# Kernel optimization log

Measured on AMD Instinct MI355X. Metric: run time of the kernel, lower is better.

The kernel has to match this reference:

```python
import jax, jax.numpy as jnp
import numpy as np

N = 50000      # num_nodes
E = 12500      # num hyperedges
NNZ = 400000   # incidence pairs
OBS = 64
LAT = 64
STEPS = 20     # (t1 - t0) / dt = 1.0 / 0.05
DT = 0.05
SQRT_DT = DT ** 0.5
SIGMA_INIT = 0.1


def setup_inputs() -> dict:
    key = jax.random.key(0)
    ks = jax.random.split(key, 12)
    w = lambda k, o, i: jax.random.normal(k, (o, i), dtype=jnp.float32) * (1.0 / np.sqrt(i))
    return {
        "x": jax.random.normal(ks[0], (N, OBS), dtype=jnp.float32),
        "enc_w1": w(ks[1], LAT, OBS),
        "enc_b1": jnp.zeros((LAT,), jnp.float32),
        "enc_w2": w(ks[2], LAT, LAT),
        "enc_b2": jnp.zeros((LAT,), jnp.float32),
        "conv_w": w(ks[3], LAT, LAT),
        "conv_b": jnp.zeros((LAT,), jnp.float32),
        "sigma": SIGMA_INIT * jnp.ones((LAT,), jnp.float32),
        "dec_w1": w(ks[4], LAT, LAT),
        "dec_b1": jnp.zeros((LAT,), jnp.float32),
        "dec_w2": w(ks[5], OBS, LAT),
        "dec_b2": jnp.zeros((OBS,), jnp.float32),
        "node_idx": jax.random.randint(ks[6], (NNZ,), 0, N),
        "edge_idx": jax.random.randint(ks[7], (NNZ,), 0, E),
        "seed": 0,
    }


def _mlp(x, w1, b1, w2, b2):
    # eqx.nn.MLP depth=1: linear -> relu -> linear, applied per node (vmapped == matmul)
    return jax.nn.relu(x @ w1.T + b1) @ w2.T + b2


def reference(x, enc_w1, enc_b1, enc_w2, enc_b2, conv_w, conv_b, sigma,
              dec_w1, dec_b1, dec_w2, dec_b2, node_idx, edge_idx, seed):
    # incidence degree normalization (HGNN-style), computed once
    ones = jnp.ones((NNZ,), jnp.float32)
    edge_deg_inv = 1.0 / jnp.maximum(jax.ops.segment_sum(ones, edge_idx, num_segments=E), 1.0)
    node_deg_inv = 1.0 / jnp.maximum(jax.ops.segment_sum(ones, node_idx, num_segments=N), 1.0)

    def conv(y):
        m = y @ conv_w.T                                                    # [N, LAT]
        e = jax.ops.segment_sum(m[node_idx], edge_idx, num_segments=E)     # node -> hyperedge
        e = e * edge_deg_inv[:, None]
        out = jax.ops.segment_sum(e[edge_idx], node_idx, num_segments=N)   # hyperedge -> node
        return out * node_deg_inv[:, None] + conv_b

    def step(y, k):
        dw = jax.random.normal(k, (N, LAT), dtype=y.dtype)
        drift = jnp.tanh(conv(y))                       # activation(conv) drift
        y = y + drift * DT + sigma * SQRT_DT * dw       # Euler-Maruyama, diagonal noise
        return y, None

    z0 = _mlp(x, enc_w1, enc_b1, enc_w2, enc_b2)        # encode (n, obs) -> (n, lat)
    keys = jax.random.split(jax.random.key(seed), STEPS)
    z1, _ = jax.lax.scan(step, z0, keys)
    return _mlp(z1, dec_w1, dec_b1, dec_w2, dec_b2)     # decode at t1
```

## Files before the change

kernel.cpp:

```cpp
#include <hip/hip_runtime.h>
#include <stdint.h>

#define N_NODES 50000
#define N_EDGES 12500
#define NNZV    400000
#define STEPS   20
#define DT_F    0.05f
#define SQRTDT_F 0.22360679774997896f

__device__ __forceinline__ float rdlf(float v, int l) {
  return __uint_as_float(__builtin_amdgcn_readlane(__float_as_uint(v), (unsigned)l));
}
__device__ __forceinline__ int rdli(int v, int l) {
  return (int)__builtin_amdgcn_readlane((unsigned)v, (unsigned)l);
}

__device__ __forceinline__ void tf2x32(uint32_t k0, uint32_t k1,
                                       uint32_t x0, uint32_t x1,
                                       uint32_t& o0, uint32_t& o1) {
  uint32_t k2 = k0 ^ k1 ^ 0x1BD11BDAu;
#define TFR(r) { x0 += x1; x1 = (x1 << (r)) | (x1 >> (32 - (r))); x1 ^= x0; }
  x0 += k0; x1 += k1;
  TFR(13) TFR(15) TFR(26) TFR(6)   x0 += k1; x1 += k2 + 1u;
  TFR(17) TFR(29) TFR(16) TFR(24)  x0 += k2; x1 += k0 + 2u;
  TFR(13) TFR(15) TFR(26) TFR(6)   x0 += k0; x1 += k1 + 3u;
  TFR(17) TFR(29) TFR(16) TFR(24)  x0 += k1; x1 += k2 + 4u;
  TFR(13) TFR(15) TFR(26) TFR(6)   x0 += k2; x1 += k0 + 5u;
#undef TFR
  o0 = x0; o1 = x1;
}

__device__ __forceinline__ float erfinv_xla(float x) {
  float w = -log1pf(-x * x);
  float p;
  if (w < 5.0f) {
    w = w - 2.5f;
    p =              2.81022636e-08f;
    p = fmaf(p, w,   3.43273939e-07f);
    p = fmaf(p, w,  -3.5233877e-06f);
    p = fmaf(p, w,  -4.39150654e-06f);
    p = fmaf(p, w,   0.00021858087f);
    p = fmaf(p, w,  -0.00125372503f);
    p = fmaf(p, w,  -0.00417768164f);
    p = fmaf(p, w,   0.246640727f);
    p = fmaf(p, w,   1.50140941f);
  } else {
    w = sqrtf(w) - 3.0f;
    p =             -0.000200214257f;
    p = fmaf(p, w,   0.000100950558f);
    p = fmaf(p, w,   0.00134934322f);
    p = fmaf(p, w,  -0.00367342844f);
    p = fmaf(p, w,   0.00573950773f);
    p = fmaf(p, w,  -0.0076224613f);
    p = fmaf(p, w,   0.00943887047f);
    p = fmaf(p, w,   1.00167406f);
    p = fmaf(p, w,   2.83297682f);
  }
  return p * x;
}

__device__ __forceinline__ float bits_to_normal(uint32_t b) {
  float f = __uint_as_float((b >> 9) | 0x3f800000u) - 1.0f;
  const float lo = -0.99999994f;
  float u = fmaf(f, 2.0f, lo);
  u = fmaxf(u, lo);
  return 1.41421356237f * erfinv_xla(u);
}

__global__ void k_keys(const int* __restrict__ seed, unsigned* __restrict__ keys) {
  int j = threadIdx.x;
  if (j < STEPS) {
    unsigned s = (unsigned)seed[0];
    unsigned o0, o1;
    tf2x32(0u, s, 0u, (unsigned)j, o0, o1);
    keys[2 * j] = o0; keys[2 * j + 1] = o1;
  }
}

__global__ void k_zero(int* __restrict__ p, int n) {
  int i = blockIdx.x * 256 + threadIdx.x;
  if (i < n) p[i] = 0;
}

__global__ void k_hist(const int* __restrict__ nidx, const int* __restrict__ eidx,
                       int* __restrict__ ecnt, int* __restrict__ ncnt) {
  int i = blockIdx.x * 256 + threadIdx.x;
  if (i < NNZV) {
    atomicAdd(&ecnt[eidx[i]], 1);
    atomicAdd(&ncnt[nidx[i]], 1);
  }
}

__global__ __launch_bounds__(256) void k_reduce(const int* __restrict__ cnt, int len,
                                                int* __restrict__ bsum) {
  __shared__ int sh[256];
  int b = blockIdx.x, tid = threadIdx.x;
  int base = b * 1024 + tid * 4;
  int s = 0;
#pragma unroll
  for (int j = 0; j < 4; ++j) {
    int i = base + j;
    if (i < len) s += cnt[i];
  }
  sh[tid] = s;
  __syncthreads();
  for (int off = 128; off > 0; off >>= 1) {
    if (tid < off) sh[tid] += sh[tid + off];
    __syncthreads();
  }
  if (tid == 0) bsum[b] = sh[0];
}

__global__ __launch_bounds__(256) void k_scanb(int* __restrict__ bsum, int nb) {
  __shared__ int sh[256];
  int tid = threadIdx.x;
  int v = (tid < nb) ? bsum[tid] : 0;
  sh[tid] = v;
  __syncthreads();
  for (int off = 1; off < 256; off <<= 1) {
    int t = (tid >= off) ? sh[tid - off] : 0;
    __syncthreads();
    sh[tid] += t;
    __syncthreads();
  }
  if (tid < nb) bsum[tid] = sh[tid] - v;
}

__global__ __launch_bounds__(256) void k_scatter(const int* __restrict__ cnt,
                                                 const int* __restrict__ bsum, int len,
                                                 int* __restrict__ start,
                                                 int* __restrict__ fill,
                                                 float* __restrict__ dinv) {
  __shared__ int sh[256];
  int b = blockIdx.x, tid = threadIdx.x;
  int base = b * 1024 + tid * 4;
  int c[4], lex[4];
  int s = 0;
#pragma unroll
  for (int j = 0; j < 4; ++j) {
    int i = base + j;
    c[j] = (i < len) ? cnt[i] : 0;
    lex[j] = s;
    s += c[j];
  }
  sh[tid] = s;
  __syncthreads();
  for (int off = 1; off < 256; off <<= 1) {
    int t = (tid >= off) ? sh[tid - off] : 0;
    __syncthreads();
    sh[tid] += t;
    __syncthreads();
  }
  int off0 = bsum[b] + sh[tid] - s;
#pragma unroll
  for (int j = 0; j < 4; ++j) {
    int i = base + j;
    if (i < len) {
      start[i] = off0 + lex[j];
      fill[i] = 0;
      dinv[i] = 1.0f / (float)(c[j] > 1 ? c[j] : 1);
    }
  }
}

__global__ void k_fill(const int* __restrict__ nidx, const int* __restrict__ eidx,
                       const int* __restrict__ estart, const int* __restrict__ nstart,
                       int* __restrict__ efill, int* __restrict__ nfill,
                       int* __restrict__ emem, int* __restrict__ nmem) {
  int i = blockIdx.x * 256 + threadIdx.x;
  if (i < NNZV) {
    int e = eidx[i], n = nidx[i];
    int pe = atomicAdd(&efill[e], 1);
    emem[estart[e] + pe] = n;
    int pn = atomicAdd(&nfill[n], 1);
    nmem[nstart[n] + pn] = e;
  }
}

__device__ __forceinline__ void stage_swz(const float* __restrict__ w,
                                          float* __restrict__ lds, int tid) {
  for (int idx = tid; idx < 4096; idx += 256) {
    int j = idx >> 6, k = idx & 63;
    lds[k * 64 + (j ^ k)] = w[idx];
  }
}

__device__ __forceinline__ float seg_gather_sum(const float* __restrict__ rows,
                                                const int* __restrict__ mem,
                                                int start, int deg, int lane) {
  float acc0 = 0.f, acc1 = 0.f;
  for (int base = 0; base < deg; base += 64) {
    int rem = min(64, deg - base);
    int ids = (lane < rem) ? mem[start + base + lane] : 0;
    int i = 0;
    for (; i + 8 <= rem; i += 8) {
      int i0 = rdli(ids, i),     i1 = rdli(ids, i + 1);
      int i2 = rdli(ids, i + 2), i3 = rdli(ids, i + 3);
      int i4 = rdli(ids, i + 4), i5 = rdli(ids, i + 5);
      int i6 = rdli(ids, i + 6), i7 = rdli(ids, i + 7);
      float v0 = rows[(size_t)i0 * 64 + lane], v1 = rows[(size_t)i1 * 64 + lane];
      float v2 = rows[(size_t)i2 * 64 + lane], v3 = rows[(size_t)i3 * 64 + lane];
      float v4 = rows[(size_t)i4 * 64 + lane], v5 = rows[(size_t)i5 * 64 + lane];
      float v6 = rows[(size_t)i6 * 64 + lane], v7 = rows[(size_t)i7 * 64 + lane];
      acc0 += (v0 + v1) + (v2 + v3);
      acc1 += (v4 + v5) + (v6 + v7);
    }
    for (; i + 4 <= rem; i += 4) {
      int i0 = rdli(ids, i),     i1 = rdli(ids, i + 1);
      int i2 = rdli(ids, i + 2), i3 = rdli(ids, i + 3);
      float v0 = rows[(size_t)i0 * 64 + lane], v1 = rows[(size_t)i1 * 64 + lane];
      float v2 = rows[(size_t)i2 * 64 + lane], v3 = rows[(size_t)i3 * 64 + lane];
      acc0 += (v0 + v1) + (v2 + v3);
    }
    for (; i < rem; ++i) acc0 += rows[(size_t)rdli(ids, i) * 64 + lane];
  }
  return acc0 + acc1;
}

__global__ __launch_bounds__(256) void k_encoder(
    const float* __restrict__ x, const float* __restrict__ w1,
    const float* __restrict__ b1, const float* __restrict__ w2,
    const float* __restrict__ b2, float* __restrict__ y) {
  __shared__ float lw1[4096], lw2[4096];
  int tid = threadIdx.x;
  stage_swz(w1, lw1, tid);
  stage_swz(w2, lw2, tid);
  __syncthreads();
  int lane = tid & 63, wave = tid >> 6;
  float w1r[64], w2r[64];
#pragma unroll
  for (int k = 0; k < 64; ++k) {
    w1r[k] = lw1[k * 64 + (lane ^ k)];
    w2r[k] = lw2[k * 64 + (lane ^ k)];
  }
  float b1v = b1[lane], b2v = b2[lane];
  int gw = blockIdx.x * 4 + wave, nw = gridDim.x * 4;
  for (int n = gw; n < N_NODES; n += nw) {
    float xv = x[(size_t)n * 64 + lane];
    float a0 = 0.f, a1 = 0.f, a2 = 0.f, a3 = 0.f;
#pragma unroll
    for (int k = 0; k < 64; k += 4) {
      a0 = fmaf(rdlf(xv, k),     w1r[k],     a0);
      a1 = fmaf(rdlf(xv, k + 1), w1r[k + 1], a1);
      a2 = fmaf(rdlf(xv, k + 2), w1r[k + 2], a2);
      a3 = fmaf(rdlf(xv, k + 3), w1r[k + 3], a3);
    }
    float h = fmaxf((a0 + a1) + (a2 + a3) + b1v, 0.f);
    a0 = a1 = a2 = a3 = 0.f;
#pragma unroll
    for (int k = 0; k < 64; k += 4) {
      a0 = fmaf(rdlf(h, k),     w2r[k],     a0);
      a1 = fmaf(rdlf(h, k + 1), w2r[k + 1], a1);
      a2 = fmaf(rdlf(h, k + 2), w2r[k + 2], a2);
      a3 = fmaf(rdlf(h, k + 3), w2r[k + 3], a3);
    }
    y[(size_t)n * 64 + lane] = (a0 + a1) + (a2 + a3) + b2v;
  }
}

__global__ __launch_bounds__(256) void k_edge(
    const float* __restrict__ y, float* __restrict__ e,
    const int* __restrict__ estart, const int* __restrict__ ecnt,
    const int* __restrict__ emem, const float* __restrict__ edinv,
    const float* __restrict__ cw) {
  __shared__ float lcw[4096];
  int tid = threadIdx.x;
  stage_swz(cw, lcw, tid);
  __syncthreads();
  int lane = tid & 63, wave = tid >> 6;
  float cwr[64];
#pragma unroll
  for (int k = 0; k < 64; ++k) cwr[k] = lcw[k * 64 + (lane ^ k)];
  int gw = blockIdx.x * 4 + wave, nw = gridDim.x * 4;
  for (int ed = gw; ed < N_EDGES; ed += nw) {
    int start = estart[ed], deg = ecnt[ed];
    float acc = seg_gather_sum(y, emem, start, deg, lane);
    float a0 = 0.f, a1 = 0.f, a2 = 0.f, a3 = 0.f;
#pragma unroll
    for (int k = 0; k < 64; k += 4) {
      a0 = fmaf(rdlf(acc, k),     cwr[k],     a0);
      a1 = fmaf(rdlf(acc, k + 1), cwr[k + 1], a1);
      a2 = fmaf(rdlf(acc, k + 2), cwr[k + 2], a2);
      a3 = fmaf(rdlf(acc, k + 3), cwr[k + 3], a3);
    }
    e[(size_t)ed * 64 + lane] = ((a0 + a1) + (a2 + a3)) * edinv[ed];
  }
}

__global__ __launch_bounds__(256) void k_node(
    const float* __restrict__ e, float* __restrict__ y,
    const int* __restrict__ nstart, const int* __restrict__ ncnt,
    const int* __restrict__ nmem, const float* __restrict__ ndinv,
    const float* __restrict__ cb, const float* __restrict__ sigma,
    const unsigned* __restrict__ keys, int s) {
  int tid = threadIdx.x;
  int lane = tid & 63, wave = tid >> 6;
  float cbv = cb[lane];
  float sgv = sigma[lane] * SQRTDT_F;
  unsigned ka = keys[2 * s], kb = keys[2 * s + 1];
  int gw = blockIdx.x * 4 + wave, nw = gridDim.x * 4;
  for (int n = gw; n < N_NODES; n += nw) {
    uint32_t r0, r1;
    tf2x32(ka, kb, 0u, (unsigned)(n * 64 + lane), r0, r1);
    float dw = bits_to_normal(r0 ^ r1);
    float acc = seg_gather_sum(e, nmem, nstart[n], ncnt[n], lane);
    float yv = y[(size_t)n * 64 + lane];
    yv = yv + tanhf(fmaf(acc, ndinv[n], cbv)) * DT_F + sgv * dw;
    y[(size_t)n * 64 + lane] = yv;
  }
}

__global__ __launch_bounds__(256) void k_decoder(
    const float* __restrict__ y, const float* __restrict__ w1,
    const float* __restrict__ b1, const float* __restrict__ w2,
    const float* __restrict__ b2, float* __restrict__ out) {
  __shared__ float lw1[4096], lw2[4096];
  int tid = threadIdx.x;
  stage_swz(w1, lw1, tid);
  stage_swz(w2, lw2, tid);
  __syncthreads();
  int lane = tid & 63, wave = tid >> 6;
  float w1r[64], w2r[64];
#pragma unroll
  for (int k = 0; k < 64; ++k) {
    w1r[k] = lw1[k * 64 + (lane ^ k)];
    w2r[k] = lw2[k * 64 + (lane ^ k)];
  }
  float b1v = b1[lane], b2v = b2[lane];
  int gw = blockIdx.x * 4 + wave, nw = gridDim.x * 4;
  for (int n = gw; n < N_NODES; n += nw) {
    float xv = y[(size_t)n * 64 + lane];
    float a0 = 0.f, a1 = 0.f, a2 = 0.f, a3 = 0.f;
#pragma unroll
    for (int k = 0; k < 64; k += 4) {
      a0 = fmaf(rdlf(xv, k),     w1r[k],     a0);
      a1 = fmaf(rdlf(xv, k + 1), w1r[k + 1], a1);
      a2 = fmaf(rdlf(xv, k + 2), w1r[k + 2], a2);
      a3 = fmaf(rdlf(xv, k + 3), w1r[k + 3], a3);
    }
    float h = fmaxf((a0 + a1) + (a2 + a3) + b1v, 0.f);
    a0 = a1 = a2 = a3 = 0.f;
#pragma unroll
    for (int k = 0; k < 64; k += 4) {
      a0 = fmaf(rdlf(h, k),     w2r[k],     a0);
      a1 = fmaf(rdlf(h, k + 1), w2r[k + 1], a1);
      a2 = fmaf(rdlf(h, k + 2), w2r[k + 2], a2);
      a3 = fmaf(rdlf(h, k + 3), w2r[k + 3], a3);
    }
    out[(size_t)n * 64 + lane] = (a0 + a1) + (a2 + a3) + b2v;
  }
}

extern "C" void kernel_launch(void* const* d_in, const int* in_sizes, int n_in,
                              void* d_out, int out_size, void* d_ws, size_t ws_size,
                              hipStream_t stream) {
  (void)in_sizes; (void)n_in; (void)out_size; (void)ws_size;
  const float* x      = (const float*)d_in[0];
  const float* enc_w1 = (const float*)d_in[1];
  const float* enc_b1 = (const float*)d_in[2];
  const float* enc_w2 = (const float*)d_in[3];
  const float* enc_b2 = (const float*)d_in[4];
  const float* conv_w = (const float*)d_in[5];
  const float* conv_b = (const float*)d_in[6];
  const float* sigma  = (const float*)d_in[7];
  const float* dec_w1 = (const float*)d_in[8];
  const float* dec_b1 = (const float*)d_in[9];
  const float* dec_w2 = (const float*)d_in[10];
  const float* dec_b2 = (const float*)d_in[11];
  const int* node_idx = (const int*)d_in[12];
  const int* edge_idx = (const int*)d_in[13];
  const int* seed     = (const int*)d_in[14];

  char* wsb = (char*)d_ws;
  size_t off = 0;
  auto alloc = [&](size_t bytes) -> void* {
    void* p = wsb + off;
    off = (off + bytes + 255) & ~(size_t)255;
    return p;
  };
  float* y        = (float*)alloc((size_t)N_NODES * 64 * 4);
  float* e        = (float*)alloc((size_t)N_EDGES * 64 * 4);
  int* edge_cnt   = (int*)alloc((size_t)N_EDGES * 4);
  int* node_cnt   = (int*)alloc((size_t)N_NODES * 4);
  int* edge_start = (int*)alloc((size_t)N_EDGES * 4);
  int* node_start = (int*)alloc((size_t)N_NODES * 4);
  int* edge_fill  = (int*)alloc((size_t)N_EDGES * 4);
  int* node_fill  = (int*)alloc((size_t)N_NODES * 4);
  int* edge_mem   = (int*)alloc((size_t)NNZV * 4);
  int* node_mem   = (int*)alloc((size_t)NNZV * 4);
  float* edinv    = (float*)alloc((size_t)N_EDGES * 4);
  float* ndinv    = (float*)alloc((size_t)N_NODES * 4);
  unsigned* keys  = (unsigned*)alloc(2 * STEPS * 4);
  int* ebsum      = (int*)alloc(256 * 4);
  int* nbsum      = (int*)alloc(256 * 4);

  const int EB = (N_EDGES + 1023) / 1024;
  const int NB = (N_NODES + 1023) / 1024;

  dim3 b256(256);
  hipLaunchKernelGGL(k_keys, dim3(1), dim3(64), 0, stream, seed, keys);
  hipLaunchKernelGGL(k_zero, dim3((N_EDGES + 255) / 256), b256, 0, stream, edge_cnt, N_EDGES);
  hipLaunchKernelGGL(k_zero, dim3((N_NODES + 255) / 256), b256, 0, stream, node_cnt, N_NODES);
  hipLaunchKernelGGL(k_hist, dim3((NNZV + 255) / 256), b256, 0, stream,
                     node_idx, edge_idx, edge_cnt, node_cnt);
  hipLaunchKernelGGL(k_reduce, dim3(EB), b256, 0, stream, edge_cnt, N_EDGES, ebsum);
  hipLaunchKernelGGL(k_reduce, dim3(NB), b256, 0, stream, node_cnt, N_NODES, nbsum);
  hipLaunchKernelGGL(k_scanb, dim3(1), b256, 0, stream, ebsum, EB);
  hipLaunchKernelGGL(k_scanb, dim3(1), b256, 0, stream, nbsum, NB);
  hipLaunchKernelGGL(k_scatter, dim3(EB), b256, 0, stream,
                     edge_cnt, ebsum, N_EDGES, edge_start, edge_fill, edinv);
  hipLaunchKernelGGL(k_scatter, dim3(NB), b256, 0, stream,
                     node_cnt, nbsum, N_NODES, node_start, node_fill, ndinv);
  hipLaunchKernelGGL(k_fill, dim3((NNZV + 255) / 256), b256, 0, stream,
                     node_idx, edge_idx, edge_start, node_start,
                     edge_fill, node_fill, edge_mem, node_mem);
  hipLaunchKernelGGL(k_encoder, dim3(1024), b256, 0, stream,
                     x, enc_w1, enc_b1, enc_w2, enc_b2, y);
  for (int s = 0; s < STEPS; ++s) {
    hipLaunchKernelGGL(k_edge, dim3(1024), b256, 0, stream,
                       y, e, edge_start, edge_cnt, edge_mem, edinv, conv_w);
    hipLaunchKernelGGL(k_node, dim3(2048), b256, 0, stream,
                       e, y, node_start, node_cnt, node_mem, ndinv,
                       conv_b, sigma, keys, s);
  }
  hipLaunchKernelGGL(k_decoder, dim3(1024), b256, 0, stream,
                     y, dec_w1, dec_b1, dec_w2, dec_b2, (float*)d_out);
}
```

Baseline: 1.210 ms.

## Use fast intrinsics for erfinv/tanh, unroll gather 16-wide, reorder node loads

Swaps log1pf and tanhf for __logf/__expf-based approximations in the noise and drift paths. Widens the gather unroll from 8 to 16 loads with four accumulators to keep more memory requests in flight. Moves the y load and neighbor gather ahead of the RNG compute in k_node so memory latency can overlap the Threefry and erfinv arithmetic. The fast math may slightly change the normal samples and drift compared with the reference, and the wider unroll raises register pressure.

```diff
diff --git a/kernel.cpp b/kernel.cpp
--- a/kernel.cpp
+++ b/kernel.cpp
@@ -30,8 +30,8 @@
   o0 = x0; o1 = x1;
 }
 
-__device__ __forceinline__ float erfinv_xla(float x) {
-  float w = -log1pf(-x * x);
+__device__ __forceinline__ float erfinv_fast(float x) {
+  float w = -__logf((1.0f - x) * (1.0f + x));
   float p;
   if (w < 5.0f) {
     w = w - 2.5f;
@@ -64,7 +64,12 @@
   const float lo = -0.99999994f;
   float u = fmaf(f, 2.0f, lo);
   u = fmaxf(u, lo);
-  return 1.41421356237f * erfinv_xla(u);
+  return 1.41421356237f * erfinv_fast(u);
+}
+
+__device__ __forceinline__ float fast_tanhf(float x) {
+  float t = __expf(2.0f * x);
+  return 1.0f - 2.0f / (t + 1.0f);
 }
 
 __global__ void k_keys(const int* __restrict__ seed, unsigned* __restrict__ keys) {
@@ -188,33 +193,43 @@
 __device__ __forceinline__ float seg_gather_sum(const float* __restrict__ rows,
                                                 const int* __restrict__ mem,
                                                 int start, int deg, int lane) {
-  float acc0 = 0.f, acc1 = 0.f;
+  float acc0 = 0.f, acc1 = 0.f, acc2 = 0.f, acc3 = 0.f;
   for (int base = 0; base < deg; base += 64) {
     int rem = min(64, deg - base);
     int ids = (lane < rem) ? mem[start + base + lane] : 0;
     int i = 0;
-    for (; i + 8 <= rem; i += 8) {
-      int i0 = rdli(ids, i),     i1 = rdli(ids, i + 1);
-      int i2 = rdli(ids, i + 2), i3 = rdli(ids, i + 3);
-      int i4 = rdli(ids, i + 4), i5 = rdli(ids, i + 5);
-      int i6 = rdli(ids, i + 6), i7 = rdli(ids, i + 7);
-      float v0 = rows[(size_t)i0 * 64 + lane], v1 = rows[(size_t)i1 * 64 + lane];
-      float v2 = rows[(size_t)i2 * 64 + lane], v3 = rows[(size_t)i3 * 64 + lane];
-      float v4 = rows[(size_t)i4 * 64 + lane], v5 = rows[(size_t)i5 * 64 + lane];
-      float v6 = rows[(size_t)i6 * 64 + lane], v7 = rows[(size_t)i7 * 64 + lane];
+    for (; i + 16 <= rem; i += 16) {
+      int j0  = rdli(ids, i),      j1  = rdli(ids, i + 1);
+      int j2  = rdli(ids, i + 2),  j3  = rdli(ids, i + 3);
+      int j4  = rdli(ids, i + 4),  j5  = rdli(ids, i + 5);
+      int j6  = rdli(ids, i + 6),  j7  = rdli(ids, i + 7);
+      int j8  = rdli(ids, i + 8),  j9  = rdli(ids, i + 9);
+      int j10 = rdli(ids, i + 10), j11 = rdli(ids, i + 11);
+      int j12 = rdli(ids, i + 12), j13 = rdli(ids, i + 13);
+      int j14 = rdli(ids, i + 14), j15 = rdli(ids, i + 15);
+      float v0  = rows[(size_t)j0  * 64 + lane], v1  = rows[(size_t)j1  * 64 + lane];
+      float v2  = rows[(size_t)j2  * 64 + lane], v3  = rows[(size_t)j3  * 64 + lane];
+      float v4  = rows[(size_t)j4  * 64 + lane], v5  = rows[(size_t)j5  * 64 + lane];
+      float v6  = rows[(size_t)j6  * 64 + lane], v7  = rows[(size_t)j7  * 64 + lane];
+      float v8  = rows[(size_t)j8  * 64 + lane], v9  = rows[(size_t)j9  * 64 + lane];
+      float v10 = rows[(size_t)j10 * 64 + lane], v11 = rows[(size_t)j11 * 64 + lane];
+      float v12 = rows[(size_t)j12 * 64 + lane], v13 = rows[(size_t)j13 * 64 + lane];
+      float v14 = rows[(size_t)j14 * 64 + lane], v15 = rows[(size_t)j15 * 64 + lane];
       acc0 += (v0 + v1) + (v2 + v3);
       acc1 += (v4 + v5) + (v6 + v7);
+      acc2 += (v8 + v9) + (v10 + v11);
+      acc3 += (v12 + v13) + (v14 + v15);
     }
     for (; i + 4 <= rem; i += 4) {
-      int i0 = rdli(ids, i),     i1 = rdli(ids, i + 1);
-      int i2 = rdli(ids, i + 2), i3 = rdli(ids, i + 3);
-      float v0 = rows[(size_t)i0 * 64 + lane], v1 = rows[(size_t)i1 * 64 + lane];
-      float v2 = rows[(size_t)i2 * 64 + lane], v3 = rows[(size_t)i3 * 64 + lane];
+      int j0 = rdli(ids, i),     j1 = rdli(ids, i + 1);
+      int j2 = rdli(ids, i + 2), j3 = rdli(ids, i + 3);
+      float v0 = rows[(size_t)j0 * 64 + lane], v1 = rows[(size_t)j1 * 64 + lane];
+      float v2 = rows[(size_t)j2 * 64 + lane], v3 = rows[(size_t)j3 * 64 + lane];
       acc0 += (v0 + v1) + (v2 + v3);
     }
     for (; i < rem; ++i) acc0 += rows[(size_t)rdli(ids, i) * 64 + lane];
   }
-  return acc0 + acc1;
+  return (acc0 + acc1) + (acc2 + acc3);
 }
 
 __global__ __launch_bounds__(256) void k_encoder(
@@ -300,12 +315,12 @@
   unsigned ka = keys[2 * s], kb = keys[2 * s + 1];
   int gw = blockIdx.x * 4 + wave, nw = gridDim.x * 4;
   for (int n = gw; n < N_NODES; n += nw) {
+    float yv = y[(size_t)n * 64 + lane];
+    float acc = seg_gather_sum(e, nmem, nstart[n], ncnt[n], lane);
     uint32_t r0, r1;
     tf2x32(ka, kb, 0u, (unsigned)(n * 64 + lane), r0, r1);
     float dw = bits_to_normal(r0 ^ r1);
-    float acc = seg_gather_sum(e, nmem, nstart[n], ncnt[n], lane);
-    float yv = y[(size_t)n * 64 + lane];
-    yv = yv + tanhf(fmaf(acc, ndinv[n], cbv)) * DT_F + sgv * dw;
+    yv = fmaf(fast_tanhf(fmaf(acc, ndinv[n], cbv)), DT_F, fmaf(sgv, dw, yv));
     y[(size_t)n * 64 + lane] = yv;
   }
 }
```

Result: slower. 1.437 ms (+18.7%).

## Use scalar index loads in gathers, fast transcendentals, LDS weights, larger edge grid

Applied to the files above, without the earlier changes.

The segment gather now makes the row index wave-uniform with readfirstlane and reads neighbour indices as scalar loads, replacing the per-lane index load followed by readlane. In the edge kernel the 64-register conv weight copy is dropped and weights are read from LDS on each use, which lowers register pressure, and the edge grid is doubled. The node update switches to a fast exp-based tanh and a __logf-based erfinv, and hoists per-node loads ahead of the RNG. These approximations can move results slightly away from the reference, and the LDS reads add shared-memory traffic inside the inner product.

```diff
diff --git a/kernel.cpp b/kernel.cpp
--- a/kernel.cpp
+++ b/kernel.cpp
@@ -11,8 +11,8 @@
 __device__ __forceinline__ float rdlf(float v, int l) {
   return __uint_as_float(__builtin_amdgcn_readlane(__float_as_uint(v), (unsigned)l));
 }
-__device__ __forceinline__ int rdli(int v, int l) {
-  return (int)__builtin_amdgcn_readlane((unsigned)v, (unsigned)l);
+__device__ __forceinline__ int rfl(int v) {
+  return (int)__builtin_amdgcn_readfirstlane((unsigned)v);
 }
 
 __device__ __forceinline__ void tf2x32(uint32_t k0, uint32_t k1,
@@ -30,8 +30,8 @@
   o0 = x0; o1 = x1;
 }
 
-__device__ __forceinline__ float erfinv_xla(float x) {
-  float w = -log1pf(-x * x);
+__device__ __forceinline__ float erfinv_fast(float x) {
+  float w = -__logf((1.0f - x) * (1.0f + x));
   float p;
   if (w < 5.0f) {
     w = w - 2.5f;
@@ -64,7 +64,12 @@
   const float lo = -0.99999994f;
   float u = fmaf(f, 2.0f, lo);
   u = fmaxf(u, lo);
-  return 1.41421356237f * erfinv_xla(u);
+  return 1.41421356237f * erfinv_fast(u);
+}
+
+__device__ __forceinline__ float fast_tanhf(float x) {
+  float t = __expf(2.0f * x);
+  return 1.0f - 2.0f / (t + 1.0f);
 }
 
 __global__ void k_keys(const int* __restrict__ seed, unsigned* __restrict__ keys) {
@@ -185,36 +190,25 @@
   }
 }
 
-__device__ __forceinline__ float seg_gather_sum(const float* __restrict__ rows,
-                                                const int* __restrict__ mem,
-                                                int start, int deg, int lane) {
-  float acc0 = 0.f, acc1 = 0.f;
-  for (int base = 0; base < deg; base += 64) {
-    int rem = min(64, deg - base);
-    int ids = (lane < rem) ? mem[start + base + lane] : 0;
-    int i = 0;
-    for (; i + 8 <= rem; i += 8) {
-      int i0 = rdli(ids, i),     i1 = rdli(ids, i + 1);
-      int i2 = rdli(ids, i + 2), i3 = rdli(ids, i + 3);
-      int i4 = rdli(ids, i + 4), i5 = rdli(ids, i + 5);
-      int i6 = rdli(ids, i + 6), i7 = rdli(ids, i + 7);
-      float v0 = rows[(size_t)i0 * 64 + lane], v1 = rows[(size_t)i1 * 64 + lane];
-      float v2 = rows[(size_t)i2 * 64 + lane], v3 = rows[(size_t)i3 * 64 + lane];
-      float v4 = rows[(size_t)i4 * 64 + lane], v5 = rows[(size_t)i5 * 64 + lane];
-      float v6 = rows[(size_t)i6 * 64 + lane], v7 = rows[(size_t)i7 * 64 + lane];
-      acc0 += (v0 + v1) + (v2 + v3);
-      acc1 += (v4 + v5) + (v6 + v7);
-    }
-    for (; i + 4 <= rem; i += 4) {
-      int i0 = rdli(ids, i),     i1 = rdli(ids, i + 1);
-      int i2 = rdli(ids, i + 2), i3 = rdli(ids, i + 3);
-      float v0 = rows[(size_t)i0 * 64 + lane], v1 = rows[(size_t)i1 * 64 + lane];
-      float v2 = rows[(size_t)i2 * 64 + lane], v3 = rows[(size_t)i3 * 64 + lane];
-      acc0 += (v0 + v1) + (v2 + v3);
-    }
-    for (; i < rem; ++i) acc0 += rows[(size_t)rdli(ids, i) * 64 + lane];
-  }
-  return acc0 + acc1;
+__device__ __forceinline__ float seg_gather_scalar(const float* __restrict__ rows,
+                                                   const int* __restrict__ mem,
+                                                   int st, int deg, int lane) {
+  float a0 = 0.f, a1 = 0.f, a2 = 0.f, a3 = 0.f;
+  int i = 0;
+  for (; i + 8 <= deg; i += 8) {
+    int d0 = mem[st + i],     d1 = mem[st + i + 1];
+    int d2 = mem[st + i + 2], d3 = mem[st + i + 3];
+    int d4 = mem[st + i + 4], d5 = mem[st + i + 5];
+    int d6 = mem[st + i + 6], d7 = mem[st + i + 7];
+    float v0 = rows[(size_t)d0 * 64 + lane], v1 = rows[(size_t)d1 * 64 + lane];
+    float v2 = rows[(size_t)d2 * 64 + lane], v3 = rows[(size_t)d3 * 64 + lane];
+    float v4 = rows[(size_t)d4 * 64 + lane], v5 = rows[(size_t)d5 * 64 + lane];
+    float v6 = rows[(size_t)d6 * 64 + lane], v7 = rows[(size_t)d7 * 64 + lane];
+    a0 += v0 + v1; a1 += v2 + v3; a2 += v4 + v5; a3 += v6 + v7;
+  }
+  for (; i < deg; ++i)
+    a0 += rows[(size_t)mem[st + i] * 64 + lane];
+  return (a0 + a1) + (a2 + a3);
 }
 
 __global__ __launch_bounds__(256) void k_encoder(
@@ -268,22 +262,21 @@
   stage_swz(cw, lcw, tid);
   __syncthreads();
   int lane = tid & 63, wave = tid >> 6;
-  float cwr[64];
-#pragma unroll
-  for (int k = 0; k < 64; ++k) cwr[k] = lcw[k * 64 + (lane ^ k)];
   int gw = blockIdx.x * 4 + wave, nw = gridDim.x * 4;
   for (int ed = gw; ed < N_EDGES; ed += nw) {
-    int start = estart[ed], deg = ecnt[ed];
-    float acc = seg_gather_sum(y, emem, start, deg, lane);
+    int edu = rfl(ed);
+    int st  = estart[edu], deg = ecnt[edu];
+    float div = edinv[edu];
+    float acc = seg_gather_scalar(y, emem, st, deg, lane);
     float a0 = 0.f, a1 = 0.f, a2 = 0.f, a3 = 0.f;
 #pragma unroll
     for (int k = 0; k < 64; k += 4) {
-      a0 = fmaf(rdlf(acc, k),     cwr[k],     a0);
-      a1 = fmaf(rdlf(acc, k + 1), cwr[k + 1], a1);
-      a2 = fmaf(rdlf(acc, k + 2), cwr[k + 2], a2);
-      a3 = fmaf(rdlf(acc, k + 3), cwr[k + 3], a3);
-    }
-    e[(size_t)ed * 64 + lane] = ((a0 + a1) + (a2 + a3)) * edinv[ed];
+      a0 = fmaf(rdlf(acc, k),     lcw[k * 64 + (lane ^ k)],             a0);
+      a1 = fmaf(rdlf(acc, k + 1), lcw[(k + 1) * 64 + (lane ^ (k + 1))], a1);
+      a2 = fmaf(rdlf(acc, k + 2), lcw[(k + 2) * 64 + (lane ^ (k + 2))], a2);
+      a3 = fmaf(rdlf(acc, k + 3), lcw[(k + 3) * 64 + (lane ^ (k + 3))], a3);
+    }
+    e[(size_t)edu * 64 + lane] = ((a0 + a1) + (a2 + a3)) * div;
   }
 }
 
@@ -300,13 +293,16 @@
   unsigned ka = keys[2 * s], kb = keys[2 * s + 1];
   int gw = blockIdx.x * 4 + wave, nw = gridDim.x * 4;
   for (int n = gw; n < N_NODES; n += nw) {
+    int nu = rfl(n);
+    int st = nstart[nu], deg = ncnt[nu];
+    float dinv = ndinv[nu];
+    float yv = y[(size_t)nu * 64 + lane];
+    float acc = seg_gather_scalar(e, nmem, st, deg, lane);
     uint32_t r0, r1;
-    tf2x32(ka, kb, 0u, (unsigned)(n * 64 + lane), r0, r1);
+    tf2x32(ka, kb, 0u, (unsigned)(nu * 64 + lane), r0, r1);
     float dw = bits_to_normal(r0 ^ r1);
-    float acc = seg_gather_sum(e, nmem, nstart[n], ncnt[n], lane);
-    float yv = y[(size_t)n * 64 + lane];
-    yv = yv + tanhf(fmaf(acc, ndinv[n], cbv)) * DT_F + sgv * dw;
-    y[(size_t)n * 64 + lane] = yv;
+    yv = fmaf(fast_tanhf(fmaf(acc, dinv, cbv)), DT_F, fmaf(sgv, dw, yv));
+    y[(size_t)nu * 64 + lane] = yv;
   }
 }
 
@@ -417,7 +413,7 @@
   hipLaunchKernelGGL(k_encoder, dim3(1024), b256, 0, stream,
                      x, enc_w1, enc_b1, enc_w2, enc_b2, y);
   for (int s = 0; s < STEPS; ++s) {
-    hipLaunchKernelGGL(k_edge, dim3(1024), b256, 0, stream,
+    hipLaunchKernelGGL(k_edge, dim3(2048), b256, 0, stream,
                        y, e, edge_start, edge_cnt, edge_mem, edinv, conv_w);
     hipLaunchKernelGGL(k_node, dim3(2048), b256, 0, stream,
                        e, y, node_start, node_cnt, node_mem, ndinv,
```

Measured after the change: 1.079 ms. 1.12x faster.
